# Kernel tuning notes

Hardware: AMD Instinct MI355X
Metric: run time of the kernel (lower is better)

## Reference

```python
import jax, jax.numpy as jnp
from jax import lax
import numpy as np


def _pool_matrix(L, S):
    # AdaptiveAvgPool1d(L -> S): output i averages input [floor(i*L/S), ceil((i+1)*L/S))
    P = np.zeros((S, L), dtype=np.float32)
    for i in range(S):
        s = (i * L) // S
        e = -(-((i + 1) * L) // S)
        P[i, s:e] = 1.0 / (e - s)
    return jnp.asarray(P)


def _gmask_index(Lc, kind):
    idx = jnp.arange(Lc, dtype=jnp.float32)
    ref = float((Lc + 1) // 2 if kind == 'center' else Lc - 1)
    sigma = jnp.mean(jnp.abs(idx - ref))
    w = jnp.exp(-0.5 * (idx - ref) ** 2 / sigma ** 2)
    return w / w.sum()  # (Lc,)


def _gmask_vector(seq, kind):
    Lc = seq.shape[1]
    ref_i = (Lc + 1) // 2 if kind == 'center' else Lc - 1
    diff = seq - seq[:, ref_i, :][:, None, :]
    d = jnp.sqrt(jnp.maximum(jnp.sum(diff * diff, axis=2), 1e-12))  # safe ||.||2
    sigma = jnp.mean(d, axis=1, keepdims=True)
    w = jnp.exp(-0.5 * (d / sigma) ** 2)
    return w / jnp.sum(w, axis=1, keepdims=True)  # (B, Lc)


def _l2norm(w):  # F.normalize(p=2, dim=1)
    return w / jnp.maximum(jnp.linalg.norm(w, axis=1, keepdims=True), 1e-12)


def _dwconv(u, w, b, L):
    # u: (B, len, C); depthwise Conv1d, padding=d_conv-1 both sides, slice [:, :, :L]
    C = u.shape[-1]
    pad = w.shape[-1] - 1
    v = lax.conv_general_dilated(u.transpose(0, 2, 1), w, (1,), [(pad, pad)],
                                 dimension_numbers=('NCH', 'OIH', 'NCH'),
                                 feature_group_count=C)
    v = v + b[None, :, None]
    return v[:, :, :L].transpose(0, 2, 1)


def _ssm(u, W_xp, b_xp, W_dt, b_dt, A_log, D):
    d_state = A_log.shape[1]
    dt_rank = W_dt.shape[1]
    A = -jnp.exp(A_log)                                       # (d_inner, d_state)
    dbc = u @ W_xp.T + b_xp
    dr = dbc[..., :dt_rank]
    Bm = dbc[..., dt_rank:dt_rank + d_state]
    Cm = dbc[..., dt_rank + d_state:]
    delta = jax.nn.softplus(dr @ W_dt.T + b_dt)               # (B, L, d_inner)
    deltaA = jnp.exp(delta[..., None] * A)                    # (B, L, d_inner, d_state)
    BX = (delta * u)[..., None] * Bm[:, :, None, :]           # (B, L, d_inner, d_state)

    def comb(e1, e2):  # h_t = a_t * h_{t-1} + b_t (parallel scan)
        a1, b1 = e1
        a2, b2 = e2
        return a1 * a2, a2 * b1 + b2

    hs = lax.associative_scan(comb, (deltaA, BX), axis=1)[1]
    return jnp.einsum('blds,bls->bld', hs, Cm) + D * u


def _forward(x, W_in_x, W_in_z, conv_w_f, conv_b_f, conv_w_b, conv_b_b,
             W_xp_f, b_xp_f, W_dt_f, b_dt_f, A_log_f, D_f,
             W_xp_b, b_xp_b, W_dt_b, b_dt_b, A_log_b, D_b,
             W_pro_to, b_pro_to, token_wA, token_wV, W_out):
    B, L, Dm = x.shape
    S = token_wA.shape[1]
    xi = x @ W_in_x.T
    z = x @ W_in_z.T
    mid = L // 2 + 1
    x_f = xi[:, :mid]
    x_b = xi[:, mid - 1:][:, ::-1]
    x_f = jax.nn.silu(_dwconv(x_f, conv_w_f, conv_b_f, L))
    x_b = jax.nn.silu(_dwconv(x_b, conv_w_b, conv_b_b, L))
    y_f = _ssm(x_f, W_xp_f, b_xp_f, W_dt_f, b_dt_f, A_log_f, D_f)
    y_b = _ssm(x_b, W_xp_b, b_xp_b, W_dt_b, b_dt_b, A_log_b, D_b)
    Lc = y_f.shape[1]
    m_f = _l2norm(_gmask_index(Lc, 'last')[None, :] * _gmask_vector(y_f, 'last'))
    m_b = _l2norm(_gmask_index(Lc, 'last')[None, :] * _gmask_vector(y_b, 'last'))
    y_cat = jnp.concatenate([y_f * m_f[..., None], y_b * m_b[:, ::-1, None]], axis=-1)
    y = y_cat @ W_pro_to.T + b_pro_to
    m = _l2norm(_gmask_index(Lc, 'center')[None, :] * _gmask_vector(y, 'center'))
    y = y * m[..., None]
    # tokenizer (direction 'f'), dropout is identity at eval
    Atok = jax.nn.softmax(jnp.einsum('bld,td->btl', y, token_wA[0]), axis=-1)
    VV = jnp.einsum('bld,de->ble', y, token_wV[0])
    T = jnp.einsum('btl,ble->bte', Atok, VV)
    # z branch: adaptive avg pool L -> S then silu
    P = _pool_matrix(L, S)
    zp = jax.nn.silu(jnp.einsum('bld,sl->bsd', z, P))
    return (T * zp) @ W_out.T


def setup_inputs() -> dict:
    key = jax.random.key(0)
    B, L, D = 8, 2049, 256
    d_inner, d_state, dt_rank, d_conv, S = 512, 16, 16, 4, 64
    ks = jax.random.split(key, 20)
    rn = lambda k, sh, sc: jax.random.normal(k, sh, jnp.float32) * sc
    A_log = jnp.tile(jnp.log(jnp.arange(1.0, d_state + 1.0, dtype=jnp.float32))[None, :], (d_inner, 1))
    return {
        'x': rn(ks[0], (B, L, D), 1.0),
        'W_in_x': rn(ks[1], (d_inner, D), D ** -0.5),
        'W_in_z': rn(ks[2], (d_inner, D), D ** -0.5),
        'conv_w_f': rn(ks[3], (d_inner, 1, d_conv), 0.5),
        'conv_b_f': rn(ks[4], (d_inner,), 0.1),
        'conv_w_b': rn(ks[5], (d_inner, 1, d_conv), 0.5),
        'conv_b_b': rn(ks[6], (d_inner,), 0.1),
        'W_xp_f': rn(ks[7], (dt_rank + 2 * d_state, d_inner), d_inner ** -0.5),
        'b_xp_f': rn(ks[8], (dt_rank + 2 * d_state,), 0.02),
        'W_dt_f': rn(ks[9], (d_inner, dt_rank), dt_rank ** -0.5),
        'b_dt_f': jax.random.uniform(ks[10], (d_inner,), jnp.float32, -4.0, -2.0),
        'A_log_f': A_log,
        'D_f': jnp.ones((d_inner,), jnp.float32),
        'W_xp_b': rn(ks[11], (dt_rank + 2 * d_state, d_inner), d_inner ** -0.5),
        'b_xp_b': rn(ks[12], (dt_rank + 2 * d_state,), 0.02),
        'W_dt_b': rn(ks[13], (d_inner, dt_rank), dt_rank ** -0.5),
        'b_dt_b': jax.random.uniform(ks[14], (d_inner,), jnp.float32, -4.0, -2.0),
        'A_log_b': A_log,
        'D_b': jnp.ones((d_inner,), jnp.float32),
        'W_pro_to': rn(ks[15], (d_inner, 2 * d_inner), (2 * d_inner) ** -0.5),
        'b_pro_to': jnp.zeros((d_inner,), jnp.float32),
        'token_wA': rn(ks[16], (1, S, d_inner), (2.0 / d_inner) ** 0.5),
        'token_wV': rn(ks[17], (1, d_inner, d_inner), (2.0 / d_inner) ** 0.5),
        'W_out': rn(ks[18], (D, d_inner), d_inner ** -0.5),
    }


def reference(x, W_in_x, W_in_z, conv_w_f, conv_b_f, conv_w_b, conv_b_b,
              W_xp_f, b_xp_f, W_dt_f, b_dt_f, A_log_f, D_f,
              W_xp_b, b_xp_b, W_dt_b, b_dt_b, A_log_b, D_b,
              W_pro_to, b_pro_to, token_wA, token_wV, W_out):
    return _forward(x, W_in_x, W_in_z, conv_w_f, conv_b_f, conv_w_b, conv_b_b,
                    W_xp_f, b_xp_f, W_dt_f, b_dt_f, A_log_f, D_f,
                    W_xp_b, b_xp_b, W_dt_b, b_dt_b, A_log_b, D_b,
                    W_pro_to, b_pro_to, token_wA, token_wV, W_out)
```

## Files before the change

kernel.cpp:

```cpp
#include <hip/hip_runtime.h>
#include <math.h>

#define BB 8
#define LL 2049
#define DD 256
#define EE 512
#define NS 16
#define LC 1028
#define SS 64
#define SC 64
#define CH 17
#define LN2F 0.6931471805599453f

typedef __attribute__((ext_vector_type(8))) short short8x;
typedef __attribute__((ext_vector_type(4))) float f32x4;

__device__ __forceinline__ float4 ld4g(const float* p) { return *(const float4*)p; }

__device__ __forceinline__ unsigned short bfrne(float f)
{
    unsigned int u = __float_as_uint(f);
    unsigned int r = (u + 0x7FFFu + ((u >> 16) & 1u)) >> 16;
    return (unsigned short)r;
}

__device__ __forceinline__ float bf2f(unsigned short u)
{
    return __uint_as_float((unsigned int)u << 16);
}

__device__ __forceinline__ float fast_softplus(float x)
{
    float sp = __log2f(1.f + __expf(x)) * LN2F;
    return x > 8.f ? x + __expf(-x) : sp;
}

__device__ __forceinline__ float fast_silu(float x)
{
    return __fdividef(x, 1.f + __expf(-x));
}

__device__ __forceinline__ void gl_lds16(const unsigned short* g, unsigned short* l)
{
    __builtin_amdgcn_global_load_lds(
        (const __attribute__((address_space(1))) unsigned int*)g,
        (__attribute__((address_space(3))) unsigned int*)l, 16, 0, 0);
}

template<bool OBF>
__device__ __forceinline__ void gemm_bf16_core(
    unsigned short* As, unsigned short* Bs,
    const unsigned short* __restrict__ A, const unsigned short* __restrict__ Bw,
    const float* __restrict__ bias, void* __restrict__ C,
    int M, int N, int K, int ldc)
{
    const int tid = threadIdx.x;
    const int wave = tid >> 6, lane = tid & 63;
    const int quad = lane >> 4, l16 = lane & 15;
    const int m0 = blockIdx.y * 128, n0 = blockIdx.x * 128;
    const int wm = (wave >> 1) * 64, wn = (wave & 1) * 64;
    const int srow = lane >> 2;
    const int skoff = (lane & 3) * 8;

    f32x4 acc[4][4];
#pragma unroll
    for (int i = 0; i < 4; i++)
#pragma unroll
        for (int j = 0; j < 4; j++) { f32x4 z = {0.f, 0.f, 0.f, 0.f}; acc[i][j] = z; }

    for (int k0 = 0; k0 < K; k0 += 32) {
#pragma unroll
        for (int half = 0; half < 2; half++) {
            int r = wave * 32 + half * 16 + srow;
            int ga = m0 + r; if (ga > M - 1) ga = M - 1;
            int gb = n0 + r; if (gb > N - 1) gb = N - 1;
            gl_lds16(A + (size_t)ga * K + k0 + skoff, &As[(wave * 32 + half * 16) * 32]);
            gl_lds16(Bw + (size_t)gb * K + k0 + skoff, &Bs[(wave * 32 + half * 16) * 32]);
        }
        __syncthreads();
        short8x af[4], bf[4];
#pragma unroll
        for (int t = 0; t < 4; t++) {
            af[t] = *(const short8x*)&As[(wm + t * 16 + l16) * 32 + quad * 8];
            bf[t] = *(const short8x*)&Bs[(wn + t * 16 + l16) * 32 + quad * 8];
        }
#pragma unroll
        for (int mt = 0; mt < 4; mt++)
#pragma unroll
            for (int nt = 0; nt < 4; nt++)
                acc[mt][nt] = __builtin_amdgcn_mfma_f32_16x16x32_bf16(
                    af[mt], bf[nt], acc[mt][nt], 0, 0, 0);
        __syncthreads();
    }

#pragma unroll
    for (int mt = 0; mt < 4; mt++) {
#pragma unroll
        for (int r = 0; r < 4; r++) {
            int m = m0 + wm + mt * 16 + quad * 4 + r;
            if (m >= M) continue;
#pragma unroll
            for (int nt = 0; nt < 4; nt++) {
                int n = n0 + wn + nt * 16 + l16;
                if (n >= N) continue;
                float v = acc[mt][nt][r];
                if (bias) v += bias[n];
                if (OBF) ((unsigned short*)C)[(size_t)m * ldc + n] = bfrne(v);
                else     ((float*)C)[(size_t)m * ldc + n] = v;
            }
        }
    }
}

__global__ __launch_bounds__(256) void gemm_bf16_bt(
    const unsigned short* __restrict__ A, const unsigned short* __restrict__ Bw,
    const float* __restrict__ bias, float* __restrict__ C,
    int M, int N, int K, int ldc)
{
    __shared__ unsigned short As[128 * 32];
    __shared__ unsigned short Bs[128 * 32];
    gemm_bf16_core<false>(As, Bs, A, Bw, bias, C, M, N, K, ldc);
}

__global__ __launch_bounds__(256) void gemm_bf16_bt_obf(
    const unsigned short* __restrict__ A, const unsigned short* __restrict__ Bw,
    const float* __restrict__ bias, unsigned short* __restrict__ C,
    int M, int N, int K, int ldc)
{
    __shared__ unsigned short As[128 * 32];
    __shared__ unsigned short Bs[128 * 32];
    gemm_bf16_core<true>(As, Bs, A, Bw, bias, C, M, N, K, ldc);
}

__global__ __launch_bounds__(256) void gemm_bf16_pair(
    const unsigned short* __restrict__ A0, const unsigned short* __restrict__ A1,
    const unsigned short* __restrict__ B0, const unsigned short* __restrict__ B1,
    const float* __restrict__ bias0, const float* __restrict__ bias1,
    float* __restrict__ C0, float* __restrict__ C1,
    int M, int N, int K, int ldc)
{
    __shared__ unsigned short As[128 * 32];
    __shared__ unsigned short Bs[128 * 32];
    int z = blockIdx.z;
    gemm_bf16_core<false>(As, Bs, z ? A1 : A0, z ? B1 : B0, z ? bias1 : bias0,
                          z ? C1 : C0, M, N, K, ldc);
}

__global__ __launch_bounds__(256) void gemm_bf16_pair_obf(
    const unsigned short* __restrict__ A0, const unsigned short* __restrict__ A1,
    const unsigned short* __restrict__ B0, const unsigned short* __restrict__ B1,
    unsigned short* __restrict__ C0, unsigned short* __restrict__ C1,
    int M, int N, int K, int ldc)
{
    __shared__ unsigned short As[128 * 32];
    __shared__ unsigned short Bs[128 * 32];
    int z = blockIdx.z;
    gemm_bf16_core<true>(As, Bs, z ? A1 : A0, z ? B1 : B0, nullptr,
                         z ? C1 : C0, M, N, K, ldc);
}

__global__ __launch_bounds__(256) void cvt_all(
    const float* __restrict__ s0, unsigned short* __restrict__ d0,
    const float* __restrict__ s1, unsigned short* __restrict__ d1,
    const float* __restrict__ s2, unsigned short* __restrict__ d2,
    const float* __restrict__ s3, unsigned short* __restrict__ d3,
    const float* __restrict__ s4, unsigned short* __restrict__ d4,
    const float* __restrict__ s5, unsigned short* __restrict__ d5,
    const float* __restrict__ s6, unsigned short* __restrict__ d6,
    const float* __restrict__ sV, unsigned short* __restrict__ dV)
{
    __shared__ float tile[32][33];
    if (blockIdx.x < 1024) {
        const size_t c0 = 1049088, c1 = c0 + 32768, c2 = c1 + 32768, c3 = c2 + 6144,
                     c4 = c3 + 6144, c5 = c4 + 131072, c6 = c5 + 8192;
        size_t stride = (size_t)1024 * 256;
        for (size_t i = (size_t)blockIdx.x * 256 + threadIdx.x; i < c6; i += stride) {
            const float* s; unsigned short* d; size_t j;
            if (i < c0)      { s = s0; d = d0; j = i; }
            else if (i < c1) { s = s1; d = d1; j = i - c0; }
            else if (i < c2) { s = s2; d = d2; j = i - c1; }
            else if (i < c3) { s = s3; d = d3; j = i - c2; }
            else if (i < c4) { s = s4; d = d4; j = i - c3; }
            else if (i < c5) { s = s5; d = d5; j = i - c4; }
            else             { s = s6; d = d6; j = i - c5; }
            float4 v = ((const float4*)s)[j];
            ushort4 o;
            o.x = bfrne(v.x); o.y = bfrne(v.y); o.z = bfrne(v.z); o.w = bfrne(v.w);
            ((ushort4*)d)[j] = o;
        }
    } else {
        int t = blockIdx.x - 1024;
        int bx = t & 15, by = t >> 4;
        int tx = threadIdx.x & 31, ty = threadIdx.x >> 5;
        for (int i = 0; i < 32; i += 8)
            tile[ty + i][tx] = sV[(size_t)(by * 32 + ty + i) * 512 + bx * 32 + tx];
        __syncthreads();
        for (int i = 0; i < 32; i += 8)
            dV[(size_t)(bx * 32 + ty + i) * 512 + by * 32 + tx] = bfrne(tile[tx][ty + i]);
    }
}

__global__ __launch_bounds__(256) void gemm_abt(
    const float* __restrict__ A, const float* __restrict__ Bw,
    const float* __restrict__ bias, float* __restrict__ C,
    float* __restrict__ Cpart, int M, int N, int K)
{
    __shared__ float As[16][132];
    __shared__ float Bs[16][132];
    const int tid = threadIdx.x;
    const int tx = tid & 15, ty = tid >> 4;
    const int m0 = blockIdx.y * 128, n0 = blockIdx.x * 128;
    const int Ks = K / gridDim.z;
    const int kbeg = blockIdx.z * Ks, kend = kbeg + Ks;
    const int r0 = tid >> 2, r1 = r0 + 64;
    const int kc = (tid & 3) * 4;

    float acc[8][8];
#pragma unroll
    for (int i = 0; i < 8; i++)
#pragma unroll
        for (int j = 0; j < 8; j++) acc[i][j] = 0.f;

    const float4 z4 = make_float4(0.f, 0.f, 0.f, 0.f);
    float4 a0, a1, b0, b1;
    a0 = (m0 + r0 < M) ? ld4g(A + (size_t)(m0 + r0) * K + kbeg + kc) : z4;
    a1 = (m0 + r1 < M) ? ld4g(A + (size_t)(m0 + r1) * K + kbeg + kc) : z4;
    b0 = (n0 + r0 < N) ? ld4g(Bw + (size_t)(n0 + r0) * K + kbeg + kc) : z4;
    b1 = (n0 + r1 < N) ? ld4g(Bw + (size_t)(n0 + r1) * K + kbeg + kc) : z4;

    for (int k0 = kbeg; k0 < kend; k0 += 16) {
        As[kc + 0][r0] = a0.x; As[kc + 1][r0] = a0.y; As[kc + 2][r0] = a0.z; As[kc + 3][r0] = a0.w;
        As[kc + 0][r1] = a1.x; As[kc + 1][r1] = a1.y; As[kc + 2][r1] = a1.z; As[kc + 3][r1] = a1.w;
        Bs[kc + 0][r0] = b0.x; Bs[kc + 1][r0] = b0.y; Bs[kc + 2][r0] = b0.z; Bs[kc + 3][r0] = b0.w;
        Bs[kc + 0][r1] = b1.x; Bs[kc + 1][r1] = b1.y; Bs[kc + 2][r1] = b1.z; Bs[kc + 3][r1] = b1.w;
        __syncthreads();
        if ((k0 + 16) < kend) {
            int kn = k0 + 16 + kc;
            a0 = (m0 + r0 < M) ? ld4g(A + (size_t)(m0 + r0) * K + kn) : z4;
            a1 = (m0 + r1 < M) ? ld4g(A + (size_t)(m0 + r1) * K + kn) : z4;
            b0 = (n0 + r0 < N) ? ld4g(Bw + (size_t)(n0 + r0) * K + kn) : z4;
            b1 = (n0 + r1 < N) ? ld4g(Bw + (size_t)(n0 + r1) * K + kn) : z4;
        }
#pragma unroll
        for (int kk = 0; kk < 16; kk++) {
            float4 alo = *(const float4*)&As[kk][ty * 4];
            float4 ahi = *(const float4*)&As[kk][64 + ty * 4];
            float4 blo = *(const float4*)&Bs[kk][tx * 4];
            float4 bhi = *(const float4*)&Bs[kk][64 + tx * 4];
            float a[8] = {alo.x, alo.y, alo.z, alo.w, ahi.x, ahi.y, ahi.z, ahi.w};
            float b[8] = {blo.x, blo.y, blo.z, blo.w, bhi.x, bhi.y, bhi.z, bhi.w};
#pragma unroll
            for (int i = 0; i < 8; i++)
#pragma unroll
                for (int j = 0; j < 8; j++) acc[i][j] += a[i] * b[j];
        }
        __syncthreads();
    }

    float* Co = (blockIdx.z == 0) ? C : Cpart + (size_t)(blockIdx.z - 1) * M * N;
    const bool addb = (bias != nullptr) && (blockIdx.z == 0);
#pragma unroll
    for (int i = 0; i < 8; i++) {
        int m = m0 + (i < 4 ? ty * 4 + i : 64 + ty * 4 + i - 4);
        if (m >= M) continue;
#pragma unroll
        for (int jh = 0; jh < 2; jh++) {
            int n = n0 + jh * 64 + tx * 4;
            if (n >= N) continue;
            float4 o;
            o.x = acc[i][jh * 4 + 0]; o.y = acc[i][jh * 4 + 1];
            o.z = acc[i][jh * 4 + 2]; o.w = acc[i][jh * 4 + 3];
            if (addb) {
                o.x += bias[n]; o.y += bias[n + 1];
                o.z += bias[n + 2]; o.w += bias[n + 3];
            }
            *(float4*)(Co + (size_t)m * N + n) = o;
        }
    }
}

__global__ __launch_bounds__(256) void reduce_add(
    float* __restrict__ C, const float* __restrict__ P, int parts, size_t total)
{
    size_t stride = (size_t)gridDim.x * 256 * 4;
    for (size_t i = ((size_t)blockIdx.x * 256 + threadIdx.x) * 4; i < total; i += stride) {
        float4 c = *(float4*)(C + i);
        for (int p = 0; p < parts; p++) {
            float4 v = *(const float4*)(P + (size_t)p * total + i);
            c.x += v.x; c.y += v.y; c.z += v.z; c.w += v.w;
        }
        *(float4*)(C + i) = c;
    }
}

__global__ __launch_bounds__(256) void conv_silu_kernel(
    const unsigned short* __restrict__ xi,
    const float* __restrict__ wf, const float* __restrict__ bf,
    const float* __restrict__ wb, const float* __restrict__ bbk,
    unsigned short* __restrict__ xfcbf, unsigned short* __restrict__ xbcbf)
{
    int idx = blockIdx.x * 256 + threadIdx.x;
    if (idx >= LC * (EE / 4)) return;
    int b = blockIdx.y;
    int dir = blockIdx.z;
    int t = idx >> 7;
    int e0 = (idx & 127) * 4;
    const float* w = dir ? wb : wf;
    float4 w0 = *(const float4*)(w + (e0 + 0) * 4);
    float4 w1 = *(const float4*)(w + (e0 + 1) * 4);
    float4 w2 = *(const float4*)(w + (e0 + 2) * 4);
    float4 w3 = *(const float4*)(w + (e0 + 3) * 4);
    float4 bias = *(const float4*)((dir ? bbk : bf) + e0);
    float s0 = bias.x, s1 = bias.y, s2 = bias.z, s3 = bias.w;
#pragma unroll
    for (int k = 0; k < 4; k++) {
        int j = t + k - 3;
        if (j >= 0 && j <= 1024) {
            int src_l = dir ? (2048 - j) : j;
            ushort4 u4 = *(const ushort4*)(xi + ((size_t)b * LL + src_l) * EE + e0);
            float wk0 = (k == 0) ? w0.x : (k == 1) ? w0.y : (k == 2) ? w0.z : w0.w;
            float wk1 = (k == 0) ? w1.x : (k == 1) ? w1.y : (k == 2) ? w1.z : w1.w;
            float wk2 = (k == 0) ? w2.x : (k == 1) ? w2.y : (k == 2) ? w2.z : w2.w;
            float wk3 = (k == 0) ? w3.x : (k == 1) ? w3.y : (k == 2) ? w3.z : w3.w;
            s0 += wk0 * bf2f(u4.x);
            s1 += wk1 * bf2f(u4.y);
            s2 += wk2 * bf2f(u4.z);
            s3 += wk3 * bf2f(u4.w);
        }
    }
    ushort4 o;
    o.x = bfrne(fast_silu(s0)); o.y = bfrne(fast_silu(s1));
    o.z = bfrne(fast_silu(s2)); o.w = bfrne(fast_silu(s3));
    *(ushort4*)((dir ? xbcbf : xfcbf) + ((size_t)b * LC + t) * EE + e0) = o;
}

__device__ __forceinline__ void pow_tree(float r, float* pw)
{
    float r2 = r * r;
    float r4 = r2 * r2;
    float r8 = r4 * r4;
    pw[0] = r;        pw[1] = r2;       pw[2] = r2 * r;   pw[3] = r4;
    pw[4] = r4 * r;   pw[5] = r4 * r2;  pw[6] = r4 * pw[2]; pw[7] = r8;
    pw[8] = r8 * r;   pw[9] = r8 * r2;  pw[10] = r8 * pw[2]; pw[11] = r8 * r4;
    pw[12] = r8 * pw[4]; pw[13] = r8 * pw[5]; pw[14] = r8 * pw[6]; pw[15] = r8 * r8;
}

__global__ __launch_bounds__(256) void scan_phase1(
    const unsigned short* __restrict__ xfc, const unsigned short* __restrict__ xbc,
    const float* __restrict__ dbcf, const float* __restrict__ dbcb,
    const float* __restrict__ Wdt_f, const float* __restrict__ bdt_f,
    const float* __restrict__ Alog_f,
    const float* __restrict__ Wdt_b, const float* __restrict__ bdt_b,
    const float* __restrict__ Alog_b,
    unsigned short* __restrict__ Hloc, float* __restrict__ Dsum,
    unsigned short* __restrict__ deltab)
{
    const int bid = blockIdx.x;
    const int half = bid & 1;
    const int c = (bid >> 1) % SC;
    const int rest = (bid >> 1) / SC;
    const int b = rest & 7;
    const int dir = rest >> 3;
    const int e = half * 256 + threadIdx.x;

    const unsigned short* u = dir ? xbc : xfc;
    const float* dbc  = dir ? dbcb : dbcf;
    const float* Wdt  = dir ? Wdt_b : Wdt_f;
    const float* bdt  = dir ? bdt_b : bdt_f;
    const float* Alog = dir ? Alog_b : Alog_f;

    float W[16], h[16];
#pragma unroll
    for (int i = 0; i < 16; i += 4) {
        float4 w4 = *(const float4*)(Wdt + e * 16 + i);
        W[i] = w4.x; W[i + 1] = w4.y; W[i + 2] = w4.z; W[i + 3] = w4.w;
    }
#pragma unroll
    for (int i = 0; i < 16; i++) h[i] = 0.f;
    float A0 = -__expf(Alog[e * 16]);
    float bd = bdt[e];
    float dsum = 0.f;

    const int l0 = c * CH;
    int l1 = l0 + CH; if (l1 > LC) l1 = LC;
    const unsigned short* urow = u + ((size_t)b * LC + l0) * EE + e;
    const float* row  = dbc + ((size_t)b * LC + l0) * 48;
    unsigned short* drow = deltab + (((size_t)dir * 8 + b) * LC + l0) * 512 + e;

    for (int l = l0; l < l1; ++l, row += 48, urow += EE, drow += 512) {
        float p = bd;
#pragma unroll
        for (int k = 0; k < 16; k++) p += row[k] * W[k];
        unsigned short dq = bfrne(fast_softplus(p));
        *drow = dq;
        float delta = bf2f(dq);
        dsum += delta;
        float du = delta * bf2f(*urow);
        float r = __expf(delta * A0);
        float pw[16];
        pow_tree(r, pw);
#pragma unroll
        for (int n = 0; n < 16; n++) h[n] = pw[n] * h[n] + du * row[16 + n];
    }
    size_t base = ((((size_t)dir * 8 + b) * SC + c) * 16) * 512 + e;
#pragma unroll
    for (int n = 0; n < 16; n++) Hloc[base + (size_t)n * 512] = bfrne(h[n]);
    Dsum[(((size_t)dir * 8 + b) * SC + c) * 512 + e] = dsum;
}

__global__ __launch_bounds__(256) void scan_phase2(
    unsigned short* __restrict__ Hloc, const float* __restrict__ Dsum,
    const float* __restrict__ Alog_f, const float* __restrict__ Alog_b)
{
    int gid = blockIdx.x * 256 + threadIdx.x;
    int e = gid & 511;
    int n = (gid >> 9) & 15;
    int b = (gid >> 13) & 7;
    int dir = gid >> 16;
    const float* Alog = dir ? Alog_b : Alog_f;
    float An = -__expf(Alog[e * 16 + n]);
    size_t base = (((size_t)dir * 8 + b) * SC * 16 + n) * 512 + e;
    size_t dbase = ((size_t)dir * 8 + b) * SC * 512 + e;
    float h = 0.f;
#pragma unroll
    for (int c = 0; c < SC; c++) {
        size_t off = base + (size_t)c * 16 * 512;
        float tmp = bf2f(Hloc[off]);
        float P = __expf(Dsum[dbase + (size_t)c * 512] * An);
        Hloc[off] = bfrne(h);
        h = P * h + tmp;
    }
}

__global__ __launch_bounds__(256) void scan_phase3(
    const unsigned short* __restrict__ xfc, const unsigned short* __restrict__ xbc,
    const float* __restrict__ dbcf, const float* __restrict__ dbcb,
    const float* __restrict__ Alog_f, const float* __restrict__ Df,
    const float* __restrict__ Alog_b, const float* __restrict__ Db,
    const unsigned short* __restrict__ Hin,
    const unsigned short* __restrict__ deltab,
    unsigned short* __restrict__ yf, unsigned short* __restrict__ yb)
{
    const int bid = blockIdx.x;
    const int half = bid & 1;
    const int c = (bid >> 1) % SC;
    const int rest = (bid >> 1) / SC;
    const int b = rest & 7;
    const int dir = rest >> 3;
    const int e = half * 256 + threadIdx.x;

    const unsigned short* u = dir ? xbc : xfc;
    const float* dbc  = dir ? dbcb : dbcf;
    const float* Alog = dir ? Alog_b : Alog_f;
    const float* Dp   = dir ? Db : Df;
    unsigned short* y = dir ? yb : yf;

    float h[16];
    float A0 = -__expf(Alog[e * 16]);
    float Dv = Dp[e];
    size_t hbase = ((((size_t)dir * 8 + b) * SC + c) * 16) * 512 + e;
#pragma unroll
    for (int n = 0; n < 16; n++) h[n] = bf2f(Hin[hbase + (size_t)n * 512]);

    const int l0 = c * CH;
    int l1 = l0 + CH; if (l1 > LC) l1 = LC;
    const unsigned short* urow = u + ((size_t)b * LC + l0) * EE + e;
    unsigned short* yrow      = y + ((size_t)b * LC + l0) * EE + e;
    const float* row  = dbc + ((size_t)b * LC + l0) * 48 + 16;
    const unsigned short* drow = deltab + (((size_t)dir * 8 + b) * LC + l0) * 512 + e;

    for (int l = l0; l < l1; ++l, row += 48, urow += EE, yrow += EE, drow += 512) {
        float delta = bf2f(*drow);
        float uv = bf2f(*urow);
        float du = delta * uv;
        float r = __expf(delta * A0);
        float pw[16];
        pow_tree(r, pw);
        float q0 = 0.f, q1 = 0.f, q2 = 0.f, q3 = 0.f;
#pragma unroll
        for (int i = 0; i < 4; i++) {
#pragma unroll
            for (int j = 0; j < 4; j++) {
                int n = i * 4 + j;
                h[n] = pw[n] * h[n] + du * row[n];
            }
            q0 += h[i * 4 + 0] * row[16 + i * 4 + 0];
            q1 += h[i * 4 + 1] * row[16 + i * 4 + 1];
            q2 += h[i * 4 + 2] * row[16 + i * 4 + 2];
            q3 += h[i * 4 + 3] * row[16 + i * 4 + 3];
        }
        *yrow = bfrne(((q0 + q1) + (q2 + q3)) + Dv * uv);
    }
}

__global__ __launch_bounds__(256) void dist2_kernel(
    const unsigned short* __restrict__ Y0, const unsigned short* __restrict__ Y1,
    float* __restrict__ D0, float* __restrict__ D1, int ref_l)
{
    const unsigned short* Y = blockIdx.z ? Y1 : Y0;
    float* dbuf = blockIdx.z ? D1 : D0;
    int wave = threadIdx.x >> 6;
    int lane = threadIdx.x & 63;
    int l = blockIdx.x * 4 + wave;
    int b = blockIdx.y;
    if (l >= LC) return;
    const unsigned short* row = Y + ((size_t)b * LC + l) * EE + lane * 8;
    const unsigned short* ref = Y + ((size_t)b * LC + ref_l) * EE + lane * 8;
    float s = 0.f;
#pragma unroll
    for (int i = 0; i < 8; i += 4) {
        ushort4 a = *(const ushort4*)(row + i);
        ushort4 r = *(const ushort4*)(ref + i);
        float dx = bf2f(a.x) - bf2f(r.x), dy = bf2f(a.y) - bf2f(r.y);
        float dz = bf2f(a.z) - bf2f(r.z), dw = bf2f(a.w) - bf2f(r.w);
        s += dx * dx + dy * dy + dz * dz + dw * dw;
    }
    for (int m = 1; m < 64; m <<= 1) s += __shfl_xor(s, m, 64);
    if (lane == 0) dbuf[(size_t)b * LC + l] = sqrtf(fmaxf(s, 1e-12f));
}

__device__ __forceinline__ float block_reduce_sum256(float v, float* red)
{
    int tid = threadIdx.x;
    red[tid] = v; __syncthreads();
    for (int s = 128; s > 0; s >>= 1) {
        if (tid < s) red[tid] += red[tid + s];
        __syncthreads();
    }
    float r = red[0]; __syncthreads();
    return r;
}

__global__ __launch_bounds__(256) void mask_finalize2(
    const float* __restrict__ db0, const float* __restrict__ db1,
    float* __restrict__ mb0, float* __restrict__ mb1, float ref)
{
    __shared__ float red[256];
    int b = blockIdx.x, tid = threadIdx.x;
    const float* d = (blockIdx.y ? db1 : db0) + (size_t)b * LC;
    float* m = (blockIdx.y ? mb1 : mb0) + (size_t)b * LC;
    float s1 = 0.f, s2 = 0.f;
    for (int l = tid; l < LC; l += 256) {
        s1 += d[l];
        s2 += fabsf((float)l - ref);
    }
    float sigma = block_reduce_sum256(s1, red) / (float)LC;
    float si    = block_reduce_sum256(s2, red) / (float)LC;
    float invsg = 1.f / sigma, invsi = 1.f / si;
    float s3 = 0.f, s4 = 0.f;
    for (int l = tid; l < LC; l += 256) {
        float t1 = d[l] * invsg;             s3 += __expf(-0.5f * t1 * t1);
        float t2 = ((float)l - ref) * invsi; s4 += __expf(-0.5f * t2 * t2);
    }
    float invwv = 1.f / block_reduce_sum256(s3, red);
    float invwi = 1.f / block_reduce_sum256(s4, red);
    float s5 = 0.f;
    for (int l = tid; l < LC; l += 256) {
        float t1 = d[l] * invsg;             float gv = __expf(-0.5f * t1 * t1) * invwv;
        float t2 = ((float)l - ref) * invsi; float gi = __expf(-0.5f * t2 * t2) * invwi;
        float v = gi * gv; s5 += v * v;
    }
    float invn = 1.f / fmaxf(sqrtf(block_reduce_sum256(s5, red)), 1e-12f);
    for (int l = tid; l < LC; l += 256) {
        float t1 = d[l] * invsg;             float gv = __expf(-0.5f * t1 * t1) * invwv;
        float t2 = ((float)l - ref) * invsi; float gi = __expf(-0.5f * t2 * t2) * invwi;
        m[l] = (gi * gv) * invn;
    }
}

__global__ __launch_bounds__(256) void build_ycat_bf16(
    const unsigned short* __restrict__ yf, const unsigned short* __restrict__ yb,
    const float* __restrict__ mf, const float* __restrict__ mb,
    unsigned short* __restrict__ ycat)
{
    size_t idx = (size_t)blockIdx.x * 256 + threadIdx.x;
    if (idx >= (size_t)BB * LC * 128) return;
    int e0 = (int)(idx & 127) * 4;
    size_t bl = idx >> 7;
    int l = (int)(bl % LC);
    int b = (int)(bl / LC);
    size_t rl = (size_t)b * LC + (LC - 1 - l);
    float mfv = mf[bl], mbv = mb[rl];
    ushort4 f4 = *(const ushort4*)(yf + bl * 512 + e0);
    ushort4 b4 = *(const ushort4*)(yb + bl * 512 + e0);
    ushort4 of, ob;
    of.x = bfrne(bf2f(f4.x) * mfv); of.y = bfrne(bf2f(f4.y) * mfv);
    of.z = bfrne(bf2f(f4.z) * mfv); of.w = bfrne(bf2f(f4.w) * mfv);
    ob.x = bfrne(bf2f(b4.x) * mbv); ob.y = bfrne(bf2f(b4.y) * mbv);
    ob.z = bfrne(bf2f(b4.z) * mbv); ob.w = bfrne(bf2f(b4.w) * mbv);
    *(ushort4*)(ycat + bl * 1024 + e0) = of;
    *(ushort4*)(ycat + bl * 1024 + 512 + e0) = ob;
}

__global__ __launch_bounds__(256) void softmax_l(
    float* __restrict__ logits, const float* __restrict__ mc)
{
    __shared__ float red[256];
    int b = blockIdx.x >> 6, t = blockIdx.x & 63;
    int tid = threadIdx.x;
    float* base = logits + (size_t)b * LC * 576 + t;
    const float* mcb = mc + (size_t)b * LC;
    float mx = -1e30f;
    for (int l = tid; l < LC; l += 256) mx = fmaxf(mx, base[(size_t)l * 576] * mcb[l]);
    red[tid] = mx; __syncthreads();
    for (int s = 128; s > 0; s >>= 1) {
        if (tid < s) red[tid] = fmaxf(red[tid], red[tid + s]);
        __syncthreads();
    }
    mx = red[0]; __syncthreads();
    float sum = 0.f;
    for (int l = tid; l < LC; l += 256) sum += __expf(base[(size_t)l * 576] * mcb[l] - mx);
    red[tid] = sum; __syncthreads();
    for (int s = 128; s > 0; s >>= 1) {
        if (tid < s) red[tid] += red[tid + s];
        __syncthreads();
    }
    float inv = 1.f / red[0];
    for (int l = tid; l < LC; l += 256)
        base[(size_t)l * 576] = __expf(base[(size_t)l * 576] * mcb[l] - mx) * inv;
}

__global__ __launch_bounds__(256) void t_kernel(
    const float* __restrict__ cc, const float* __restrict__ zp,
    const float* __restrict__ mc, float* __restrict__ T)
{
    __shared__ float As[16][64];
    int b = blockIdx.y;
    int e0 = blockIdx.x * 64;
    int lbeg = blockIdx.z * 65;
    int lend = lbeg + 65; if (lend > LC) lend = LC;
    int tid = threadIdx.x;
    int el = tid & 63;
    int tq = tid >> 6;
    float acc[16];
#pragma unroll
    for (int j = 0; j < 16; j++) acc[j] = 0.f;
    for (int l0 = lbeg; l0 < lend; l0 += 16) {
        int lld = tid >> 4;
        int tld = (tid & 15) * 4;
        int l = l0 + lld;
        float4 v = make_float4(0.f, 0.f, 0.f, 0.f);
        if (l < lend) {
            v = *(const float4*)(cc + ((size_t)b * LC + l) * 576 + tld);
            float m = mc[(size_t)b * LC + l];
            v.x *= m; v.y *= m; v.z *= m; v.w *= m;
        }
        *(float4*)&As[lld][tld] = v;
        __syncthreads();
        int lmax = lend - l0 < 16 ? lend - l0 : 16;
#pragma unroll
        for (int i = 0; i < 16; i += 4) {
            if (i >= lmax) break;
            const size_t cb = ((size_t)b * LC + l0 + i) * 576 + 64 + e0 + el;
            float v0 = cc[cb];
            float v1 = (i + 1 < lmax) ? cc[cb + 576] : 0.f;
            float v2 = (i + 2 < lmax) ? cc[cb + 1152] : 0.f;
            float v3 = (i + 3 < lmax) ? cc[cb + 1728] : 0.f;
#pragma unroll
            for (int j = 0; j < 16; j++) acc[j] += As[i][tq * 16 + j] * v0;
#pragma unroll
            for (int j = 0; j < 16; j++) acc[j] += As[i + 1][tq * 16 + j] * v1;
#pragma unroll
            for (int j = 0; j < 16; j++) acc[j] += As[i + 2][tq * 16 + j] * v2;
#pragma unroll
            for (int j = 0; j < 16; j++) acc[j] += As[i + 3][tq * 16 + j] * v3;
        }
        __syncthreads();
    }
#pragma unroll
    for (int j = 0; j < 16; j++) {
        size_t o = ((size_t)b * 64 + tq * 16 + j) * EE + e0 + el;
        atomicAdd(&T[o], acc[j] * zp[o]);
    }
}

__global__ __launch_bounds__(256) void zp_kernel(
    const unsigned short* __restrict__ z, float* __restrict__ zp,
    float* __restrict__ T)
{
    int s = blockIdx.x, b = blockIdx.y;
    int tid = threadIdx.x;
    {
        size_t base = ((size_t)b * SS + s) * 512;
        *(float4*)(T + base + tid * 2) = make_float4(0.f, 0.f, 0.f, 0.f);
    }
    int si = (s * LL) / SS;
    int ei = ((s + 1) * LL + SS - 1) / SS;
    float inv = 1.f / (float)(ei - si);
    for (int d = tid; d < EE; d += 256) {
        float acc = 0.f;
        for (int l = si; l < ei; l++) acc += bf2f(z[((size_t)b * LL + l) * EE + d]);
        zp[((size_t)b * SS + s) * EE + d] = fast_silu(acc * inv);
    }
}

extern "C" void kernel_launch(void* const* d_in, const int* in_sizes, int n_in,
                              void* d_out, int out_size, void* d_ws, size_t ws_size,
                              hipStream_t stream)
{
    const float* x        = (const float*)d_in[0];
    const float* W_in_x   = (const float*)d_in[1];
    const float* W_in_z   = (const float*)d_in[2];
    const float* conv_w_f = (const float*)d_in[3];
    const float* conv_b_f = (const float*)d_in[4];
    const float* conv_w_b = (const float*)d_in[5];
    const float* conv_b_b = (const float*)d_in[6];
    const float* W_xp_f   = (const float*)d_in[7];
    const float* b_xp_f   = (const float*)d_in[8];
    const float* W_dt_f   = (const float*)d_in[9];
    const float* b_dt_f   = (const float*)d_in[10];
    const float* A_log_f  = (const float*)d_in[11];
    const float* D_f      = (const float*)d_in[12];
    const float* W_xp_b   = (const float*)d_in[13];
    const float* b_xp_b   = (const float*)d_in[14];
    const float* W_dt_b   = (const float*)d_in[15];
    const float* b_dt_b   = (const float*)d_in[16];
    const float* A_log_b  = (const float*)d_in[17];
    const float* D_b      = (const float*)d_in[18];
    const float* W_pro    = (const float*)d_in[19];
    const float* b_pro    = (const float*)d_in[20];
    const float* token_wA = (const float*)d_in[21];
    const float* token_wV = (const float*)d_in[22];
    const float* W_out    = (const float*)d_in[23];
    float* out = (float*)d_out;
    float* ws  = (float*)d_ws;

    const size_t n1 = (size_t)BB * LL * EE;
    const size_t n2 = (size_t)BB * LC * EE;
    const size_t n3 = (size_t)BB * LC * 48;
    const size_t n4 = (size_t)BB * LC;
    const size_t n6 = (size_t)BB * SS * EE;
    const size_t nHl = (size_t)2 * BB * SC * 16 * 512;

    float* z_buf  = ws;
    float* xi     = z_buf + n1;
    float* xfc    = xi + n1;
    float* xbc    = xfc + n2;
    float* dbcf   = xbc + n2;
    float* dbcb   = dbcf + n3;
    float* yb_reg = dbcb + n3;
    float* y_buf  = yb_reg + n2;
    float* mf     = y_buf + n2;
    float* mb     = mf + n4;
    float* mc     = mb + n4;
    float* d1     = mc + n4;
    float* d2     = d1 + n4;
    float* T_buf  = d2 + n4;
    float* zp_buf = T_buf + n6;
    float* wA_reg = zp_buf + n6;
    float* wvt_reg = wA_reg + 16384;
    size_t need = (size_t)(wvt_reg + 131072 - ws) * sizeof(float);
    if (ws_size < need) return;

    unsigned short* xi_bf  = (unsigned short*)xi;
    unsigned short* z_bf   = (unsigned short*)z_buf;
    unsigned short* Hloc   = (unsigned short*)xi;
    float* Dsum   = xi + nHl / 2;
    float* Cc     = xi;
    unsigned short* yfbf   = (unsigned short*)xfc;
    unsigned short* ybbf   = (unsigned short*)xbc;
    unsigned short* xbf    = (unsigned short*)y_buf;
    unsigned short* xfcbf  = (unsigned short*)y_buf;
    unsigned short* xbcbf  = xfcbf + n2;
    unsigned short* y_bf   = (unsigned short*)y_buf;
    unsigned short* wbf1   = (unsigned short*)yb_reg;
    unsigned short* wbf2   = (unsigned short*)(yb_reg + 65536);
    unsigned short* wxpfbf = (unsigned short*)(yb_reg + 131072);
    unsigned short* wxpbbf = (unsigned short*)(yb_reg + 143360);
    unsigned short* deltab = (unsigned short*)yb_reg;
    unsigned short* wprobf = (unsigned short*)zp_buf;
    unsigned short* ycatbf = (unsigned short*)yb_reg;
    unsigned short* wABbf  = (unsigned short*)wA_reg;
    unsigned short* wAbf   = wABbf;
    unsigned short* wvtbf  = wABbf + 32768;

    dim3 blk(256);

    cvt_all<<<dim3(1280), blk, 0, stream>>>(
        x, xbf, W_in_x, wbf1, W_in_z, wbf2, W_xp_f, wxpfbf, W_xp_b, wxpbbf,
        W_pro, wprobf, token_wA, wAbf, token_wV, wvtbf);
    gemm_bf16_pair_obf<<<dim3(4, 129, 2), blk, 0, stream>>>(
        xbf, xbf, wbf1, wbf2, xi_bf, z_bf, BB * LL, EE, DD, EE);
    conv_silu_kernel<<<dim3(514, BB, 2), blk, 0, stream>>>(
        xi_bf, conv_w_f, conv_b_f, conv_w_b, conv_b_b, xfcbf, xbcbf);
    gemm_bf16_pair<<<dim3(1, 65, 2), blk, 0, stream>>>(
        xfcbf, xbcbf, wxpfbf, wxpbbf, b_xp_f, b_xp_b, dbcf, dbcb,
        BB * LC, 48, EE, 48);
    scan_phase1<<<dim3(2048), blk, 0, stream>>>(xfcbf, xbcbf, dbcf, dbcb,
        W_dt_f, b_dt_f, A_log_f, W_dt_b, b_dt_b, A_log_b, Hloc, Dsum, deltab);
    scan_phase2<<<dim3(512), blk, 0, stream>>>(Hloc, Dsum, A_log_f, A_log_b);
    scan_phase3<<<dim3(2048), blk, 0, stream>>>(xfcbf, xbcbf, dbcf, dbcb,
        A_log_f, D_f, A_log_b, D_b, Hloc, deltab, yfbf, ybbf);
    dist2_kernel<<<dim3(257, BB, 2), blk, 0, stream>>>(yfbf, ybbf, d1, d2, LC - 1);
    mask_finalize2<<<dim3(BB, 2), blk, 0, stream>>>(d1, d2, mf, mb, (float)(LC - 1));
    build_ycat_bf16<<<dim3(4112), blk, 0, stream>>>(yfbf, ybbf, mf, mb, ycatbf);
    gemm_bf16_bt_obf<<<dim3(4, 65), blk, 0, stream>>>(ycatbf, wprobf, b_pro, y_bf,
                                                      BB * LC, EE, 2 * EE, EE);
    dist2_kernel<<<dim3(257, BB, 1), blk, 0, stream>>>(y_bf, y_bf, d1, d1, (LC + 1) / 2);
    mask_finalize2<<<dim3(BB, 1), blk, 0, stream>>>(d1, d1, mc, mc, (float)((LC + 1) / 2));
    gemm_bf16_bt<<<dim3(5, 65), blk, 0, stream>>>(y_bf, wABbf, nullptr, Cc,
                                                  BB * LC, 576, EE, 576);
    softmax_l<<<dim3(BB * SS), blk, 0, stream>>>(Cc, mc);
    zp_kernel<<<dim3(SS, BB), blk, 0, stream>>>(z_bf, zp_buf, T_buf);
    t_kernel<<<dim3(8, BB, 16), blk, 0, stream>>>(Cc, zp_buf, mc, T_buf);
    gemm_abt<<<dim3(2, 4, 4), blk, 0, stream>>>(T_buf, W_out, nullptr, out, yb_reg, BB * SS, DD, EE);
    reduce_add<<<dim3(128), blk, 0, stream>>>(out, yb_reg, 3, (size_t)BB * SS * DD);
}
```

Measured before the change: 414.1 us.

## Reassociate token attention to apply value projection after pooling

The large projection GEMM now computes only the 64 attention-logit columns instead of the 576 logit-plus-value columns. The attention-weighted sum is taken over the bf16 activations directly, and a new small MFMA GEMM then applies the value weights and the zp gating to the pooled 512x512 result. This cuts FLOPs and memory traffic in the big GEMM and in t_kernel, at the cost of one extra launch and an extra bf16 rounding of the pooled T. The output GEMM's split-k factor is also raised from 4 to 8, with the reduction adjusted to match.

```diff
diff --git a/kernel.cpp b/kernel.cpp
--- a/kernel.cpp
+++ b/kernel.cpp
@@ -157,6 +157,75 @@
     int z = blockIdx.z;
     gemm_bf16_core<true>(As, Bs, z ? A1 : A0, z ? B1 : B0, nullptr,
                          z ? C1 : C0, M, N, K, ldc);
+}
+
+__global__ __launch_bounds__(256) void gemm_twv(
+    const float* __restrict__ Ty, const unsigned short* __restrict__ Wvt,
+    const float* __restrict__ zp, float* __restrict__ Tout)
+{
+    __shared__ unsigned short As[128 * 32];
+    __shared__ unsigned short Bs[128 * 32];
+    const int tid = threadIdx.x;
+    const int wave = tid >> 6, lane = tid & 63;
+    const int quad = lane >> 4, l16 = lane & 15;
+    const int m0 = blockIdx.y * 128, n0 = blockIdx.x * 128;
+    const int wm = (wave >> 1) * 64, wn = (wave & 1) * 64;
+    const int srow = lane >> 2;
+    const int skoff = (lane & 3) * 8;
+
+    f32x4 acc[4][4];
+#pragma unroll
+    for (int i = 0; i < 4; i++)
+#pragma unroll
+        for (int j = 0; j < 4; j++) { f32x4 z = {0.f, 0.f, 0.f, 0.f}; acc[i][j] = z; }
+
+    for (int k0 = 0; k0 < 512; k0 += 32) {
+#pragma unroll
+        for (int p = 0; p < 2; p++) {
+            int idx = p * 256 + tid;
+            int row = idx >> 2, seg = (idx & 3) * 8;
+            const float* src = Ty + (size_t)(m0 + row) * 512 + k0 + seg;
+            float4 va = ld4g(src), vb = ld4g(src + 4);
+            ushort4 oa, ob;
+            oa.x = bfrne(va.x); oa.y = bfrne(va.y); oa.z = bfrne(va.z); oa.w = bfrne(va.w);
+            ob.x = bfrne(vb.x); ob.y = bfrne(vb.y); ob.z = bfrne(vb.z); ob.w = bfrne(vb.w);
+            ushort4* dst = (ushort4*)&As[row * 32 + seg];
+            dst[0] = oa; dst[1] = ob;
+        }
+#pragma unroll
+        for (int half = 0; half < 2; half++) {
+            int gb = n0 + wave * 32 + half * 16 + srow;
+            gl_lds16(Wvt + (size_t)gb * 512 + k0 + skoff, &Bs[(wave * 32 + half * 16) * 32]);
+        }
+        __syncthreads();
+        short8x af[4], bf[4];
+#pragma unroll
+        for (int t = 0; t < 4; t++) {
+            af[t] = *(const short8x*)&As[(wm + t * 16 + l16) * 32 + quad * 8];
+            bf[t] = *(const short8x*)&Bs[(wn + t * 16 + l16) * 32 + quad * 8];
+        }
+#pragma unroll
+        for (int mt = 0; mt < 4; mt++)
+#pragma unroll
+            for (int nt = 0; nt < 4; nt++)
+                acc[mt][nt] = __builtin_amdgcn_mfma_f32_16x16x32_bf16(
+                    af[mt], bf[nt], acc[mt][nt], 0, 0, 0);
+        __syncthreads();
+    }
+
+#pragma unroll
+    for (int mt = 0; mt < 4; mt++) {
+#pragma unroll
+        for (int r = 0; r < 4; r++) {
+            int m = m0 + wm + mt * 16 + quad * 4 + r;
+#pragma unroll
+            for (int nt = 0; nt < 4; nt++) {
+                int n = n0 + wn + nt * 16 + l16;
+                size_t o = (size_t)m * 512 + n;
+                Tout[o] = acc[mt][nt][r] * zp[o];
+            }
+        }
+    }
 }
 
 __global__ __launch_bounds__(256) void cvt_all(
@@ -598,10 +667,10 @@
     __shared__ float red[256];
     int b = blockIdx.x >> 6, t = blockIdx.x & 63;
     int tid = threadIdx.x;
-    float* base = logits + (size_t)b * LC * 576 + t;
+    float* base = logits + (size_t)b * LC * 64 + t;
     const float* mcb = mc + (size_t)b * LC;
     float mx = -1e30f;
-    for (int l = tid; l < LC; l += 256) mx = fmaxf(mx, base[(size_t)l * 576] * mcb[l]);
+    for (int l = tid; l < LC; l += 256) mx = fmaxf(mx, base[(size_t)l * 64] * mcb[l]);
     red[tid] = mx; __syncthreads();
     for (int s = 128; s > 0; s >>= 1) {
         if (tid < s) red[tid] = fmaxf(red[tid], red[tid + s]);
@@ -609,7 +678,7 @@
     }
     mx = red[0]; __syncthreads();
     float sum = 0.f;
-    for (int l = tid; l < LC; l += 256) sum += __expf(base[(size_t)l * 576] * mcb[l] - mx);
+    for (int l = tid; l < LC; l += 256) sum += __expf(base[(size_t)l * 64] * mcb[l] - mx);
     red[tid] = sum; __syncthreads();
     for (int s = 128; s > 0; s >>= 1) {
         if (tid < s) red[tid] += red[tid + s];
@@ -617,12 +686,12 @@
     }
     float inv = 1.f / red[0];
     for (int l = tid; l < LC; l += 256)
-        base[(size_t)l * 576] = __expf(base[(size_t)l * 576] * mcb[l] - mx) * inv;
+        base[(size_t)l * 64] = __expf(base[(size_t)l * 64] * mcb[l] - mx) * inv;
 }
 
 __global__ __launch_bounds__(256) void t_kernel(
-    const float* __restrict__ cc, const float* __restrict__ zp,
-    const float* __restrict__ mc, float* __restrict__ T)
+    const float* __restrict__ cc, const unsigned short* __restrict__ y,
+    const float* __restrict__ mc, float* __restrict__ Ty)
 {
     __shared__ float As[16][64];
     int b = blockIdx.y;
@@ -641,7 +710,7 @@
         int l = l0 + lld;
         float4 v = make_float4(0.f, 0.f, 0.f, 0.f);
         if (l < lend) {
-            v = *(const float4*)(cc + ((size_t)b * LC + l) * 576 + tld);
+            v = *(const float4*)(cc + ((size_t)b * LC + l) * 64 + tld);
             float m = mc[(size_t)b * LC + l];
             v.x *= m; v.y *= m; v.z *= m; v.w *= m;
         }
@@ -651,11 +720,11 @@
 #pragma unroll
         for (int i = 0; i < 16; i += 4) {
             if (i >= lmax) break;
-            const size_t cb = ((size_t)b * LC + l0 + i) * 576 + 64 + e0 + el;
-            float v0 = cc[cb];
-            float v1 = (i + 1 < lmax) ? cc[cb + 576] : 0.f;
-            float v2 = (i + 2 < lmax) ? cc[cb + 1152] : 0.f;
-            float v3 = (i + 3 < lmax) ? cc[cb + 1728] : 0.f;
+            const size_t cb = ((size_t)b * LC + l0 + i) * 512 + e0 + el;
+            float v0 = bf2f(y[cb]);
+            float v1 = (i + 1 < lmax) ? bf2f(y[cb + 512]) : 0.f;
+            float v2 = (i + 2 < lmax) ? bf2f(y[cb + 1024]) : 0.f;
+            float v3 = (i + 3 < lmax) ? bf2f(y[cb + 1536]) : 0.f;
 #pragma unroll
             for (int j = 0; j < 16; j++) acc[j] += As[i][tq * 16 + j] * v0;
 #pragma unroll
@@ -670,7 +739,7 @@
 #pragma unroll
     for (int j = 0; j < 16; j++) {
         size_t o = ((size_t)b * 64 + tq * 16 + j) * EE + e0 + el;
-        atomicAdd(&T[o], acc[j] * zp[o]);
+        atomicAdd(&Ty[o], acc[j]);
     }
 }
 
@@ -682,7 +751,7 @@
     int tid = threadIdx.x;
     {
         size_t base = ((size_t)b * SS + s) * 512;
-        *(float4*)(T + base + tid * 2) = make_float4(0.f, 0.f, 0.f, 0.f);
+        *(float2*)(T + base + tid * 2) = make_float2(0.f, 0.f);
     }
     int si = (s * LL) / SS;
     int ei = ((s + 1) * LL + SS - 1) / SS;
@@ -757,6 +826,7 @@
     unsigned short* Hloc   = (unsigned short*)xi;
     float* Dsum   = xi + nHl / 2;
     float* Cc     = xi;
+    float* Tout   = xi + (1 << 20);
     unsigned short* yfbf   = (unsigned short*)xfc;
     unsigned short* ybbf   = (unsigned short*)xbc;
     unsigned short* xbf    = (unsigned short*)y_buf;
@@ -798,11 +868,12 @@
                                                       BB * LC, EE, 2 * EE, EE);
     dist2_kernel<<<dim3(257, BB, 1), blk, 0, stream>>>(y_bf, y_bf, d1, d1, (LC + 1) / 2);
     mask_finalize2<<<dim3(BB, 1), blk, 0, stream>>>(d1, d1, mc, mc, (float)((LC + 1) / 2));
-    gemm_bf16_bt<<<dim3(5, 65), blk, 0, stream>>>(y_bf, wABbf, nullptr, Cc,
-                                                  BB * LC, 576, EE, 576);
+    gemm_bf16_bt<<<dim3(1, 65), blk, 0, stream>>>(y_bf, wAbf, nullptr, Cc,
+                                                  BB * LC, 64, EE, 64);
     softmax_l<<<dim3(BB * SS), blk, 0, stream>>>(Cc, mc);
     zp_kernel<<<dim3(SS, BB), blk, 0, stream>>>(z_bf, zp_buf, T_buf);
-    t_kernel<<<dim3(8, BB, 16), blk, 0, stream>>>(Cc, zp_buf, mc, T_buf);
-    gemm_abt<<<dim3(2, 4, 4), blk, 0, stream>>>(T_buf, W_out, nullptr, out, yb_reg, BB * SS, DD, EE);
-    reduce_add<<<dim3(128), blk, 0, stream>>>(out, yb_reg, 3, (size_t)BB * SS * DD);
-}
+    t_kernel<<<dim3(8, BB, 16), blk, 0, stream>>>(Cc, y_bf, mc, T_buf);
+    gemm_twv<<<dim3(4, 4), blk, 0, stream>>>(T_buf, wvtbf, zp_buf, Tout);
+    gemm_abt<<<dim3(2, 4, 8), blk, 0, stream>>>(Tout, W_out, nullptr, out, yb_reg, BB * SS, DD, EE);
+    reduce_add<<<dim3(128), blk, 0, stream>>>(out, yb_reg, 7, (size_t)BB * SS * DD);
+}
```

After: 444.8 us. +7.4%, slower.
